# Performance work log

Measured on AMD Instinct MI355X. Metric: run time of the kernel, lower is better.

## Reference

```python
import jax, jax.numpy as jnp
import numpy as np

N_HEAD = 8
DROP_RATE = 0.1


def setup_inputs() -> dict:
    key = jax.random.key(0)
    k1, k2, k3 = jax.random.split(key, 3)
    n, c, h, w = 16, 512, 32, 32
    return {
        "x": jax.random.normal(k1, (n, c, h, w), jnp.float32),
        "qkv_w": jax.random.normal(k2, (3 * c, c), jnp.float32) * 0.02,
        "qkv_b": jnp.zeros((3 * c,), jnp.float32),
        "out_w": jax.random.normal(k3, (c, c), jnp.float32) * 0.02,
        "out_b": jnp.zeros((c,), jnp.float32),
        "dropout_enabled": 0,
    }


def reference(x, qkv_w, qkv_b, out_w, out_b, dropout_enabled):
    n, c, h, w = x.shape
    hd = c // N_HEAD  # head dim
    # fused QKV 1x1 conv == per-pixel matmul: [n, 3c, h, w]
    qkv = jnp.einsum('oc,nchw->nohw', qkv_w, x) + qkv_b[None, :, None, None]
    # [n, 3*n_head, hd, h*w] -> [n, 3*n_head, h*w, hd]
    qkv = jnp.swapaxes(qkv.reshape(n, N_HEAD * 3, hd, h * w), 2, 3)
    q, k, v = jnp.split(qkv, 3, axis=1)  # each [n, n_head, hw, hd]
    scale = hd ** (-0.25)
    att = jax.nn.softmax((q * scale) @ (jnp.swapaxes(k, 2, 3) * scale), axis=3)
    y = jnp.swapaxes(att @ v, 2, 3).reshape(n, c, h, w)
    y = jnp.einsum('oc,nchw->nohw', out_w, y) + out_b[None, :, None, None]
    # Dropout2d: drops whole (n, c) channel maps
    rate = DROP_RATE * dropout_enabled
    keep = jax.random.bernoulli(jax.random.key(42), 1.0 - rate, shape=(n, c))
    y = y * keep[..., None, None] / (1.0 - rate)
    return x + y
```

## Files before the change

### kernel.cpp

```cpp
#include <hip/hip_runtime.h>

typedef short bf16x8 __attribute__((ext_vector_type(8)));
typedef float f32x4 __attribute__((ext_vector_type(4)));
typedef float f32x16 __attribute__((ext_vector_type(16)));

#define MFMA16(a,b,c) __builtin_amdgcn_mfma_f32_16x16x32_bf16((a),(b),(c),0,0,0)
#define MFMA32(a,b,c) __builtin_amdgcn_mfma_f32_32x32x16_bf16((a),(b),(c),0,0,0)

static __device__ __forceinline__ unsigned short f2bf(float f){
  unsigned u; __builtin_memcpy(&u, &f, 4);
  u += 0x7fffu + ((u >> 16) & 1u);
  return (unsigned short)(u >> 16);
}

static __device__ __forceinline__ unsigned cvtpk(float lo, float hi){
  unsigned r;
  asm volatile("v_cvt_pk_bf16_f32 %0, %1, %2" : "=v"(r) : "v"(lo), "v"(hi));
  return r;
}
static __device__ __forceinline__ void pl32swap(unsigned &a, unsigned &b){
  asm volatile("v_permlane32_swap_b32 %0, %1" : "+v"(a), "+v"(b));
}

static __device__ __forceinline__ void gload_lds16(const void* g, void* l) {
  __builtin_amdgcn_global_load_lds(
      (__attribute__((address_space(1))) void*)g,
      (__attribute__((address_space(3))) void*)l, 16, 0, 0);
}

__global__ __launch_bounds__(256) void cvt_bf16(
    const float* __restrict__ in, unsigned short* __restrict__ out, int n) {
  int i = blockIdx.x * 256 + threadIdx.x;
  if (i < n) out[i] = f2bf(in[i]);
}

__global__ __launch_bounds__(256) void transpose_cvt(
    const float* __restrict__ in, unsigned short* __restrict__ out)
{
  __shared__ unsigned short tile[32][33];
  const long base = (long)blockIdx.z * 512 * 1024;
  const int t = threadIdx.x, tx = t & 31, ty = t >> 5;
  const int c0 = blockIdx.x * 32, r0 = blockIdx.y * 32;
  const float* ib = in + base;
#pragma unroll
  for (int i = 0; i < 4; ++i)
    tile[ty + i * 8][tx] = f2bf(ib[(long)(r0 + ty + i * 8) * 1024 + c0 + tx]);
  __syncthreads();
  unsigned short* ob = out + base;
#pragma unroll
  for (int i = 0; i < 4; ++i)
    ob[(long)(c0 + ty + i * 8) * 512 + r0 + tx] = tile[tx][ty + i * 8];
}

__global__ __launch_bounds__(256, 3) void gemm_qkv(
    const unsigned short* __restrict__ A, const unsigned short* __restrict__ B,
    unsigned short* __restrict__ qkvout, const float* __restrict__ bias)
{
  const int M = 1024, K = 512;
  __shared__ unsigned short As[128 * 64];
  __shared__ unsigned short Bs[128 * 64];
  const int t = threadIdx.x, lane = t & 63, wv = t >> 6;
  const int quad = lane >> 4, ln = lane & 15;

  const int L = blockIdx.x + 12 * blockIdx.y + 96 * blockIdx.z;
  const int v = (L & 7) * 192 + (L >> 3);
  const int m0 = ((v / 12) & 7) * 128, n0 = (v % 12) * 128;
  const long zb = v / 96;
  A += zb * (long)M * K;

  const int srow = wv * 32 + (lane >> 3);
  const int scol = ((lane & 7) * 8) ^ ((lane >> 3) * 8);

  f32x4 zero = {0.f, 0.f, 0.f, 0.f};
  f32x4 acc[4][4];
#pragma unroll
  for (int i = 0; i < 4; ++i)
#pragma unroll
    for (int j = 0; j < 4; ++j) acc[i][j] = zero;

  const int wm = (wv & 1) * 64, wn = (wv >> 1) * 64;
  const int rsw = (ln & 7) * 8;

  for (int kt = 0; kt < K; kt += 64) {
#pragma unroll
    for (int i = 0; i < 4; ++i) {
      gload_lds16(&A[(long)(m0 + srow + i * 8) * K + kt + scol],
                  &As[(wv * 32 + i * 8) * 64]);
      gload_lds16(&B[(long)(n0 + srow + i * 8) * K + kt + scol],
                  &Bs[(wv * 32 + i * 8) * 64]);
    }
    __syncthreads();
#pragma unroll
    for (int kk = 0; kk < 64; kk += 32) {
      bf16x8 a[4], b[4];
#pragma unroll
      for (int i = 0; i < 4; ++i)
        a[i] = *(const bf16x8*)&As[(wm + i * 16 + ln) * 64 + ((kk + quad * 8) ^ rsw)];
#pragma unroll
      for (int j = 0; j < 4; ++j)
        b[j] = *(const bf16x8*)&Bs[(wn + j * 16 + ln) * 64 + ((kk + quad * 8) ^ rsw)];
#pragma unroll
      for (int i = 0; i < 4; ++i)
#pragma unroll
        for (int j = 0; j < 4; ++j)
          acc[i][j] = MFMA16(a[i], b[j], acc[i][j]);
    }
    __syncthreads();
  }

#pragma unroll
  for (int j = 0; j < 4; ++j) {
    int o = n0 + wn + j * 16 + ln;
    float bb = bias[o];
    int part = o >> 9;
    int h = (o >> 6) & 7, d = o & 63;
    float qs = (part == 0) ? 0.18033688f : 1.0f;
#pragma unroll
    for (int i = 0; i < 4; ++i) {
      int p = m0 + wm + i * 16 + quad * 4;
      f32x4 vv = acc[i][j];
      if (part < 2) {
        unsigned short* dst = qkvout + (long)part * 8388608
            + ((long)(zb * 8 + h) * 1024 + p) * 64 + d;
#pragma unroll
        for (int r = 0; r < 4; ++r) dst[r * 64] = f2bf((vv[r] + bb) * qs);
      } else {
        long cidx = ((long)zb * 512 + (o - 1024)) * 1024 + p;
        ushort4 st;
        st.x = f2bf(vv[0] + bb); st.y = f2bf(vv[1] + bb);
        st.z = f2bf(vv[2] + bb); st.w = f2bf(vv[3] + bb);
        *(ushort4*)&qkvout[16777216 + cidx] = st;
      }
    }
  }
}

__global__ __launch_bounds__(256, 3) void gemm_out(
    const unsigned short* __restrict__ A, const unsigned short* __restrict__ B,
    float* __restrict__ C, const float* __restrict__ bias,
    const float* __restrict__ xin, const int* __restrict__ de_ptr)
{
  const int M = 1024, K = 512;
  __shared__ unsigned short As[128 * 64];
  __shared__ unsigned short Bs[128 * 64];
  const int t = threadIdx.x, lane = t & 63, wv = t >> 6;
  const int quad = lane >> 4, ln = lane & 15;

  const int L = blockIdx.x + 4 * blockIdx.y + 32 * blockIdx.z;
  const int v = (L & 7) * 64 + (L >> 3);
  const int m0 = ((v >> 2) & 7) * 128, n0 = (v & 3) * 128;
  const long zb = v >> 5;
  A += zb * (long)M * K;
  C += zb * 512l * M;
  xin += zb * 512l * M;

  const int srow = wv * 32 + (lane >> 3);
  const int scol = ((lane & 7) * 8) ^ ((lane >> 3) * 8);

  f32x4 zero = {0.f, 0.f, 0.f, 0.f};
  f32x4 acc[4][4];
#pragma unroll
  for (int i = 0; i < 4; ++i)
#pragma unroll
    for (int j = 0; j < 4; ++j) acc[i][j] = zero;

  const int wm = (wv & 1) * 64, wn = (wv >> 1) * 64;
  const int rsw = (ln & 7) * 8;

  for (int kt = 0; kt < K; kt += 64) {
#pragma unroll
    for (int i = 0; i < 4; ++i) {
      gload_lds16(&A[(long)(m0 + srow + i * 8) * K + kt + scol],
                  &As[(wv * 32 + i * 8) * 64]);
      gload_lds16(&B[(long)(n0 + srow + i * 8) * K + kt + scol],
                  &Bs[(wv * 32 + i * 8) * 64]);
    }
    __syncthreads();
#pragma unroll
    for (int kk = 0; kk < 64; kk += 32) {
      bf16x8 a[4], b[4];
#pragma unroll
      for (int i = 0; i < 4; ++i)
        a[i] = *(const bf16x8*)&As[(wm + i * 16 + ln) * 64 + ((kk + quad * 8) ^ rsw)];
#pragma unroll
      for (int j = 0; j < 4; ++j)
        b[j] = *(const bf16x8*)&Bs[(wn + j * 16 + ln) * 64 + ((kk + quad * 8) ^ rsw)];
#pragma unroll
      for (int i = 0; i < 4; ++i)
#pragma unroll
        for (int j = 0; j < 4; ++j)
          acc[i][j] = MFMA16(a[i], b[j], acc[i][j]);
    }
    __syncthreads();
  }

  float dscale = 1.0f / (1.0f - 0.1f * (float)de_ptr[0]);

#pragma unroll
  for (int j = 0; j < 4; ++j) {
    int o = n0 + wn + j * 16 + ln;
    float bb = bias[o];
#pragma unroll
    for (int i = 0; i < 4; ++i) {
      int p = m0 + wm + i * 16 + quad * 4;
      long cidx = (long)o * M + p;
      f32x4 vv = acc[i][j];
      float4 rx = *(const float4*)&xin[cidx];
      float4 st;
      st.x = rx.x + (vv[0] + bb) * dscale;
      st.y = rx.y + (vv[1] + bb) * dscale;
      st.z = rx.z + (vv[2] + bb) * dscale;
      st.w = rx.w + (vv[3] + bb) * dscale;
      *(float4*)&C[cidx] = st;
    }
  }
}

__global__ __launch_bounds__(256, 2) void attn_kernel(
    const unsigned short* __restrict__ q_pd, const unsigned short* __restrict__ k_pd,
    const unsigned short* __restrict__ v_cp, unsigned short* __restrict__ y_pc)
{
  __shared__ unsigned short Ks[2][128 * 64];
  __shared__ unsigned short Vs[2][64 * 128];
  const int t = threadIdx.x, lane = t & 63, wv = t >> 6;
  const int l31 = lane & 31, bh8 = (lane >> 5) * 8;
  const int qt = blockIdx.y >> 5;
  const int nh = blockIdx.x * 32 + (blockIdx.y & 31);
  const int n = nh >> 3, h = nh & 7;
  const int q0 = qt * 256;

  bf16x8 qa[2][4];
#pragma unroll
  for (int qg = 0; qg < 2; ++qg) {
    const unsigned short* qb =
        q_pd + ((long)nh * 1024 + q0 + wv * 64 + qg * 32 + l31) * 64;
#pragma unroll
    for (int ds = 0; ds < 4; ++ds)
      qa[qg][ds] = *(const bf16x8*)(qb + ds * 16 + bh8);
  }

  f32x16 zacc;
#pragma unroll
  for (int r = 0; r < 16; ++r) zacc[r] = 0.f;
  f32x16 o_acc[2][2];
  o_acc[0][0] = zacc; o_acc[0][1] = zacc; o_acc[1][0] = zacc; o_acc[1][1] = zacc;
  float l_acc[2] = {0.f, 0.f};

  const unsigned short* kg0 = k_pd + (long)nh * 1024 * 64;
  const unsigned short* vg0 = v_cp + ((long)n * 512 + h * 64) * 1024;

  const int krow = lane >> 3;
  const int kcol = ((lane & 7) * 8) ^ ((lane >> 3) * 8);
  const int vrow = lane >> 4;
  const int rsw = (lane & 7) * 8;
  const int vrsw = (l31 & 15) * 8;

#pragma unroll
  for (int i = 0; i < 4; ++i) {
    const int vr = i * 4 + vrow;
    const int vcol = ((lane & 15) ^ vr) * 8;
    gload_lds16(kg0 + (long)(wv * 32 + i * 8 + krow) * 64 + kcol,
                &Ks[0][(wv * 32 + i * 8) * 64]);
    gload_lds16(vg0 + (long)(wv * 16 + vr) * 1024 + vcol,
                &Vs[0][(wv * 16 + i * 4) * 128]);
  }
  __syncthreads();

  union U { bf16x8 v; unsigned u[4]; };
  auto sm_pack = [&](const f32x16& sv, bf16x8* paq, float& lac) {
    float e[16];
#pragma unroll
    for (int r = 0; r < 16; ++r) e[r] = __builtin_amdgcn_exp2f(sv[r]);
    float ls = 0.f;
#pragma unroll
    for (int r = 0; r < 16; ++r) ls += e[r];
    lac += ls;
    unsigned pk4[4][2];
#pragma unroll
    for (int hh = 0; hh < 4; ++hh) {
      pk4[hh][0] = cvtpk(e[4 * hh + 0], e[4 * hh + 1]);
      pk4[hh][1] = cvtpk(e[4 * hh + 2], e[4 * hh + 3]);
    }
#pragma unroll
    for (int hk = 0; hk < 2; ++hk) {
      unsigned a0 = pk4[2 * hk + 1][0], b0 = pk4[2 * hk][0];
      unsigned a1 = pk4[2 * hk + 1][1], b1 = pk4[2 * hk][1];
      pl32swap(a0, b0); pl32swap(a1, b1);
      U u; u.u[0] = b0; u.u[1] = b1; u.u[2] = a0; u.u[3] = a1;
      paq[hk] = u.v;
    }
  };

  for (int c = 0; c < 8; ++c) {
    const int cur = c & 1;
    if (c < 7) {
      const unsigned short* kg = kg0 + (long)(c + 1) * 128 * 64;
      const unsigned short* vg = vg0 + (c + 1) * 128;
      unsigned short* KsD = Ks[cur ^ 1];
      unsigned short* VsD = Vs[cur ^ 1];
#pragma unroll
      for (int i = 0; i < 4; ++i) {
        const int vr = i * 4 + vrow;
        const int vcol = ((lane & 15) ^ vr) * 8;
        gload_lds16(kg + (long)(wv * 32 + i * 8 + krow) * 64 + kcol,
                    &KsD[(wv * 32 + i * 8) * 64]);
        gload_lds16(vg + (long)(wv * 16 + vr) * 1024 + vcol,
                    &VsD[(wv * 16 + i * 4) * 128]);
      }
    }
    const unsigned short* KsC = Ks[cur];
    const unsigned short* VsC = Vs[cur];

#pragma unroll
    for (int kgi = 0; kgi < 4; ++kgi) {
      f32x16 s0 = zacc, s1 = zacc;
      __builtin_amdgcn_s_setprio(1);
#pragma unroll
      for (int ds = 0; ds < 4; ++ds) {
        bf16x8 ka = *(const bf16x8*)&KsC[(kgi * 32 + l31) * 64 + ((ds * 16 + bh8) ^ rsw)];
        s0 = MFMA32(ka, qa[0][ds], s0);
        s1 = MFMA32(ka, qa[1][ds], s1);
      }
      __builtin_amdgcn_s_setprio(0);
      bf16x8 pa[2][2];
      sm_pack(s0, pa[0], l_acc[0]);
      sm_pack(s1, pa[1], l_acc[1]);
      __builtin_amdgcn_s_setprio(1);
#pragma unroll
      for (int dg = 0; dg < 2; ++dg)
#pragma unroll
        for (int hk = 0; hk < 2; ++hk) {
          bf16x8 va = *(const bf16x8*)
              &VsC[(dg * 32 + l31) * 128 + (((kgi * 2 + hk) * 16 + bh8) ^ vrsw)];
          o_acc[dg][0] = MFMA32(va, pa[0][hk], o_acc[dg][0]);
          o_acc[dg][1] = MFMA32(va, pa[1][hk], o_acc[dg][1]);
        }
      __builtin_amdgcn_s_setprio(0);
    }
    __syncthreads();
  }

#pragma unroll
  for (int qg = 0; qg < 2; ++qg) {
    float la = l_acc[qg];
    la += __shfl_xor(la, 32);
    float linv = 1.0f / la;
    const int q = q0 + wv * 64 + qg * 32 + l31;
    unsigned short* yb = y_pc + ((long)n * 1024 + q) * 512 + h * 64;
#pragma unroll
    for (int dg = 0; dg < 2; ++dg) {
      f32x16 o = o_acc[dg][qg];
#pragma unroll
      for (int rq = 0; rq < 4; ++rq) {
        int d0 = dg * 32 + rq * 8 + (bh8 >> 1);
        ushort4 st;
        st.x = f2bf(o[rq * 4 + 0] * linv);
        st.y = f2bf(o[rq * 4 + 1] * linv);
        st.z = f2bf(o[rq * 4 + 2] * linv);
        st.w = f2bf(o[rq * 4 + 3] * linv);
        *(ushort4*)&yb[d0] = st;
      }
    }
  }
}

extern "C" void kernel_launch(void* const* d_in, const int* in_sizes, int n_in,
                              void* d_out, int out_size, void* d_ws, size_t ws_size,
                              hipStream_t stream) {
  (void)in_sizes; (void)n_in; (void)out_size; (void)ws_size;
  const float* x     = (const float*)d_in[0];
  const float* qkv_w = (const float*)d_in[1];
  const float* qkv_b = (const float*)d_in[2];
  const float* out_w = (const float*)d_in[3];
  const float* out_b = (const float*)d_in[4];
  const int* de = (const int*)d_in[5];
  float* out = (float*)d_out;
  unsigned short* ws = (unsigned short*)d_ws;

  unsigned short* xT   = ws;
  unsigned short* qkv  = ws + 8388608;
  unsigned short* y_pc = ws;
  unsigned short* wq   = ws + 33554432;
  unsigned short* wo   = wq + 786432;

  cvt_bf16<<<3072, 256, 0, stream>>>(qkv_w, wq, 786432);
  cvt_bf16<<<1024, 256, 0, stream>>>(out_w, wo, 262144);

  transpose_cvt<<<dim3(32, 16, 16), 256, 0, stream>>>(x, xT);

  gemm_qkv<<<dim3(12, 8, 16), 256, 0, stream>>>(xT, wq, qkv, qkv_b);

  attn_kernel<<<dim3(4, 128), 256, 0, stream>>>(
      qkv, qkv + 8388608, qkv + 16777216, y_pc);

  gemm_out<<<dim3(4, 8, 16), 256, 0, stream>>>(
      y_pc, wo, out, out_b, x, de);
}
```

Baseline: 191.3 us.

## Double-buffer LDS tiles in QKV and output GEMMs; stage Q/K epilogue through LDS

Both projection GEMMs now keep two LDS buffers, issuing the async global-to-LDS loads for the next K tile while MFMAs run on the current one, with one barrier per iteration. The QKV kernel's Q/K epilogue first writes the bf16 tile into LDS, then stores 16-byte vectors to global instead of scattered 2-byte stores. The doubled LDS use lowers the occupancy hint from 3 to 2 blocks per CU. With only one barrier per iteration and async LDS loads, correctness depends on the load being waited on before the barrier; if it is not, the prefetch may race with reads.

```diff
diff --git a/kernel.cpp b/kernel.cpp
--- a/kernel.cpp
+++ b/kernel.cpp
@@ -52,13 +52,12 @@
     ob[(long)(c0 + ty + i * 8) * 512 + r0 + tx] = tile[tx][ty + i * 8];
 }
 
-__global__ __launch_bounds__(256, 3) void gemm_qkv(
+__global__ __launch_bounds__(256, 2) void gemm_qkv(
     const unsigned short* __restrict__ A, const unsigned short* __restrict__ B,
     unsigned short* __restrict__ qkvout, const float* __restrict__ bias)
 {
   const int M = 1024, K = 512;
-  __shared__ unsigned short As[128 * 64];
-  __shared__ unsigned short Bs[128 * 64];
+  __shared__ unsigned short SM[4][128 * 64];
   const int t = threadIdx.x, lane = t & 63, wv = t >> 6;
   const int quad = lane >> 4, ln = lane & 15;
 
@@ -71,6 +70,16 @@
   const int srow = wv * 32 + (lane >> 3);
   const int scol = ((lane & 7) * 8) ^ ((lane >> 3) * 8);
 
+  auto stage = [&](int kt, unsigned short* Ad, unsigned short* Bd) {
+#pragma unroll
+    for (int i = 0; i < 4; ++i) {
+      gload_lds16(&A[(long)(m0 + srow + i * 8) * K + kt + scol],
+                  &Ad[(wv * 32 + i * 8) * 64]);
+      gload_lds16(&B[(long)(n0 + srow + i * 8) * K + kt + scol],
+                  &Bd[(wv * 32 + i * 8) * 64]);
+    }
+  };
+
   f32x4 zero = {0.f, 0.f, 0.f, 0.f};
   f32x4 acc[4][4];
 #pragma unroll
@@ -81,15 +90,13 @@
   const int wm = (wv & 1) * 64, wn = (wv >> 1) * 64;
   const int rsw = (ln & 7) * 8;
 
-  for (int kt = 0; kt < K; kt += 64) {
-#pragma unroll
-    for (int i = 0; i < 4; ++i) {
-      gload_lds16(&A[(long)(m0 + srow + i * 8) * K + kt + scol],
-                  &As[(wv * 32 + i * 8) * 64]);
-      gload_lds16(&B[(long)(n0 + srow + i * 8) * K + kt + scol],
-                  &Bs[(wv * 32 + i * 8) * 64]);
-    }
-    __syncthreads();
+  stage(0, SM[0], SM[2]);
+  __syncthreads();
+  for (int kt8 = 0; kt8 < 8; ++kt8) {
+    const int cur = kt8 & 1;
+    if (kt8 < 7) stage((kt8 + 1) * 64, SM[cur ^ 1], SM[2 + (cur ^ 1)]);
+    const unsigned short* As = SM[cur];
+    const unsigned short* Bs = SM[2 + cur];
 #pragma unroll
     for (int kk = 0; kk < 64; kk += 32) {
       bf16x8 a[4], b[4];
@@ -108,24 +115,44 @@
     __syncthreads();
   }
 
-#pragma unroll
-  for (int j = 0; j < 4; ++j) {
-    int o = n0 + wn + j * 16 + ln;
-    float bb = bias[o];
-    int part = o >> 9;
-    int h = (o >> 6) & 7, d = o & 63;
-    float qs = (part == 0) ? 0.18033688f : 1.0f;
-#pragma unroll
-    for (int i = 0; i < 4; ++i) {
-      int p = m0 + wm + i * 16 + quad * 4;
-      f32x4 vv = acc[i][j];
-      if (part < 2) {
-        unsigned short* dst = qkvout + (long)part * 8388608
-            + ((long)(zb * 8 + h) * 1024 + p) * 64 + d;
-#pragma unroll
-        for (int r = 0; r < 4; ++r) dst[r * 64] = f2bf((vv[r] + bb) * qs);
-      } else {
-        long cidx = ((long)zb * 512 + (o - 1024)) * 1024 + p;
+  const int part = n0 >> 9;
+  if (part < 2) {
+    const float qs = (part == 0) ? 0.18033688f : 1.0f;
+    unsigned short (*T)[136] = (unsigned short(*)[136])&SM[0][0];
+#pragma unroll
+    for (int j = 0; j < 4; ++j) {
+      const int oo = wn + j * 16 + ln;
+      const float bb = bias[n0 + oo];
+#pragma unroll
+      for (int i = 0; i < 4; ++i) {
+        const int pp = wm + i * 16 + quad * 4;
+        f32x4 vv = acc[i][j];
+#pragma unroll
+        for (int r = 0; r < 4; ++r)
+          T[pp + r][oo] = f2bf((vv[r] + bb) * qs);
+      }
+    }
+    __syncthreads();
+    unsigned short* qb = qkvout + (long)part * 8388608;
+#pragma unroll
+    for (int it = 0; it < 8; ++it) {
+      const int idx = it * 256 + t;
+      const int p = idx >> 4, c0 = (idx & 15) * 8;
+      const int og = n0 + c0;
+      const int h = (og >> 6) & 7, d = og & 63;
+      bf16x8 val = *(const bf16x8*)&T[p][c0];
+      *(bf16x8*)&qb[((long)(zb * 8 + h) * 1024 + m0 + p) * 64 + d] = val;
+    }
+  } else {
+#pragma unroll
+    for (int j = 0; j < 4; ++j) {
+      const int o = n0 + wn + j * 16 + ln;
+      const float bb = bias[o];
+#pragma unroll
+      for (int i = 0; i < 4; ++i) {
+        const int p = m0 + wm + i * 16 + quad * 4;
+        const long cidx = ((long)zb * 512 + (o - 1024)) * 1024 + p;
+        f32x4 vv = acc[i][j];
         ushort4 st;
         st.x = f2bf(vv[0] + bb); st.y = f2bf(vv[1] + bb);
         st.z = f2bf(vv[2] + bb); st.w = f2bf(vv[3] + bb);
@@ -135,14 +162,13 @@
   }
 }
 
-__global__ __launch_bounds__(256, 3) void gemm_out(
+__global__ __launch_bounds__(256, 2) void gemm_out(
     const unsigned short* __restrict__ A, const unsigned short* __restrict__ B,
     float* __restrict__ C, const float* __restrict__ bias,
     const float* __restrict__ xin, const int* __restrict__ de_ptr)
 {
   const int M = 1024, K = 512;
-  __shared__ unsigned short As[128 * 64];
-  __shared__ unsigned short Bs[128 * 64];
+  __shared__ unsigned short SM[4][128 * 64];
   const int t = threadIdx.x, lane = t & 63, wv = t >> 6;
   const int quad = lane >> 4, ln = lane & 15;
 
@@ -157,6 +183,16 @@
   const int srow = wv * 32 + (lane >> 3);
   const int scol = ((lane & 7) * 8) ^ ((lane >> 3) * 8);
 
+  auto stage = [&](int kt, unsigned short* Ad, unsigned short* Bd) {
+#pragma unroll
+    for (int i = 0; i < 4; ++i) {
+      gload_lds16(&A[(long)(m0 + srow + i * 8) * K + kt + scol],
+                  &Ad[(wv * 32 + i * 8) * 64]);
+      gload_lds16(&B[(long)(n0 + srow + i * 8) * K + kt + scol],
+                  &Bd[(wv * 32 + i * 8) * 64]);
+    }
+  };
+
   f32x4 zero = {0.f, 0.f, 0.f, 0.f};
   f32x4 acc[4][4];
 #pragma unroll
@@ -167,15 +203,13 @@
   const int wm = (wv & 1) * 64, wn = (wv >> 1) * 64;
   const int rsw = (ln & 7) * 8;
 
-  for (int kt = 0; kt < K; kt += 64) {
-#pragma unroll
-    for (int i = 0; i < 4; ++i) {
-      gload_lds16(&A[(long)(m0 + srow + i * 8) * K + kt + scol],
-                  &As[(wv * 32 + i * 8) * 64]);
-      gload_lds16(&B[(long)(n0 + srow + i * 8) * K + kt + scol],
-                  &Bs[(wv * 32 + i * 8) * 64]);
-    }
-    __syncthreads();
+  stage(0, SM[0], SM[2]);
+  __syncthreads();
+  for (int kt8 = 0; kt8 < 8; ++kt8) {
+    const int cur = kt8 & 1;
+    if (kt8 < 7) stage((kt8 + 1) * 64, SM[cur ^ 1], SM[2 + (cur ^ 1)]);
+    const unsigned short* As = SM[cur];
+    const unsigned short* Bs = SM[2 + cur];
 #pragma unroll
     for (int kk = 0; kk < 64; kk += 32) {
       bf16x8 a[4], b[4];
```

Result: faster. 186.0 us (-2.7%).
